# Optimization experiments

Hardware: AMD Instinct MI355X
Metric: run time of the kernel (lower is better)

## Reference

```python
import jax, jax.numpy as jnp
import numpy as np

B, L, E, H = 4, 512, 2048, 32
S = E // H  # head_size = 64
EXTRA_MAA, EXTRA_DECAY = 32, 64
EPS = 1e-5


def setup_inputs() -> dict:
    key = jax.random.key(0)
    ks = jax.random.split(key, 24)
    rn = lambda k, shp, s=1.0: jax.random.normal(k, shp, dtype=jnp.float32) * s
    return dict(
        x=rn(ks[0], (B, L, E)),
        state=rn(ks[1], (B, 2 + S, E), 0.1),
        ln1_w=jnp.ones((E,), jnp.float32), ln1_b=jnp.zeros((E,), jnp.float32),
        ln2_w=jnp.ones((E,), jnp.float32), ln2_b=jnp.zeros((E,), jnp.float32),
        maa_x=rn(ks[2], (E,), 0.02),
        maa_w1=rn(ks[3], (E, 5 * EXTRA_MAA), 0.02),
        maa_w2=rn(ks[4], (5, EXTRA_MAA, E), 0.02),
        maa_stack=rn(ks[5], (5, E), 0.02),          # [k,w,v,r,g] time_maa vectors
        time_decay=rn(ks[6], (E,), 0.5),
        decay_w1=rn(ks[7], (E, EXTRA_DECAY), 0.02),
        decay_w2=rn(ks[8], (EXTRA_DECAY, E), 0.02),
        faaaa=rn(ks[9], (H, S), 0.1),
        Wr=rn(ks[10], (E, E), 0.02), Wk=rn(ks[11], (E, E), 0.02),
        Wv=rn(ks[12], (E, E), 0.02), Wg=rn(ks[13], (E, E), 0.02),
        Wo=rn(ks[14], (E, E), 0.02),
        gn_w=jnp.ones((E,), jnp.float32), gn_b=jnp.zeros((E,), jnp.float32),
        ffn_maa_k=rn(ks[15], (E,), 0.02), ffn_maa_r=rn(ks[16], (E,), 0.02),
        ffn_Wk=rn(ks[17], (E, E), 0.02), ffn_Wr=rn(ks[18], (E, E), 0.02),
        ffn_Wv=rn(ks[19], (E, E), 0.02),
        i=0,
    )


def _ln(x, w, b):
    m = jnp.mean(x, axis=-1, keepdims=True)
    v = jnp.mean((x - m) ** 2, axis=-1, keepdims=True)
    return (x - m) * jax.lax.rsqrt(v + EPS) * w + b


def _token_shift(xn, prev_row):
    # sx_lerp[t] = x[t-1] - x[t], with state row as x[-1]
    first = (prev_row - xn[:, 0])[:, None]
    rest = xn[:, :-1] - xn[:, 1:]
    return jnp.concatenate([first, rest], axis=1)


def reference(x, state, ln1_w, ln1_b, ln2_w, ln2_b, maa_x, maa_w1, maa_w2,
              maa_stack, time_decay, decay_w1, decay_w2, faaaa,
              Wr, Wk, Wv, Wg, Wo, gn_w, gn_b,
              ffn_maa_k, ffn_maa_r, ffn_Wk, ffn_Wr, ffn_Wv, i):
    b, l = x.shape[0], x.shape[1]
    i0 = (2 + S) * i + 0
    i1 = (2 + S) * i + 1

    # ---- time mixing (parallel) ----
    xn = _ln(x, ln1_w, ln1_b)
    sx = _token_shift(xn, state[:, i1])
    xxx = jnp.tanh((xn + sx * maa_x) @ maa_w1).reshape(b, l, 5, 1, EXTRA_MAA)
    xxx = jnp.matmul(xxx, maa_w2).reshape(b, l, 5, E)   # [B,L,5,E]
    x5 = xn[:, :, None] + sx[:, :, None] * (maa_stack + xxx)

    w = jnp.exp(-jnp.exp(time_decay + jnp.tanh(x5[:, :, 1] @ decay_w1) @ decay_w2))
    w = w.reshape(b, l, H, S)
    r = (x5[:, :, 3] @ Wr.T).reshape(b, l, H, S)
    k = (x5[:, :, 0] @ Wk.T).reshape(b, l, H, S)
    v = (x5[:, :, 2] @ Wv.T).reshape(b, l, H, S)
    g = jax.nn.silu(x5[:, :, 4] @ Wg.T)                 # [B,L,E]

    s0 = state[:, (2 + S) * i + 2:(2 + S) * (i + 1)].reshape(b, H, S, S)
    u = faaaa[None, :, :, None]                         # [1,H,S,1]

    def step(s, rkvw):
        r_t, k_t, v_t, w_t = rkvw                      # each [B,H,S]
        a = k_t[:, :, :, None] * v_t[:, :, None, :]    # [B,H,S,S] outer product
        out = jnp.einsum('bhk,bhkd->bhd', r_t, u * a + s)
        return a + w_t[:, :, :, None] * s, out

    xs = tuple(jnp.moveaxis(t, 1, 0) for t in (r, k, v, w))
    _, outs = jax.lax.scan(step, s0, xs)               # outs [L,B,H,S]
    att = jnp.moveaxis(outs, 0, 1).reshape(b, l, E)

    # group norm over each head's channels
    a4 = att.reshape(b, l, H, S)
    m = jnp.mean(a4, axis=-1, keepdims=True)
    var = jnp.mean((a4 - m) ** 2, axis=-1, keepdims=True)
    att = ((a4 - m) * jax.lax.rsqrt(var + EPS)).reshape(b, l, E) * gn_w + gn_b
    x = x + (att * g) @ Wo.T

    # ---- channel mixing (parallel) ----
    xn2 = _ln(x, ln2_w, ln2_b)
    sx2 = _token_shift(xn2, state[:, i0])
    xk = xn2 + sx2 * ffn_maa_k
    xr = xn2 + sx2 * ffn_maa_r
    rr = jax.nn.sigmoid(xr @ ffn_Wr.T)
    kk = jnp.square(jax.nn.relu(xk @ ffn_Wk.T))
    x = x + rr * (kk @ ffn_Wv.T)
    return x
```

## Files before the change

kernel.cpp:

```cpp
#include <hip/hip_runtime.h>

#define EE 2048
#define LL 512
#define BBATCH 4
#define HH 32
#define SS 64
#define EPSF 1e-5f
static constexpr size_t NEL = (size_t)BBATCH * LL * EE;

typedef __attribute__((ext_vector_type(8))) short short8;
typedef __attribute__((ext_vector_type(4))) float f32x4;

__device__ __forceinline__ unsigned short f2bf(float f) {
  union { float f; unsigned u; } x; x.f = f;
  return (unsigned short)((x.u + 0x7fffu + ((x.u >> 16) & 1u)) >> 16);
}

__device__ __forceinline__ void gload_lds16(const unsigned short* g, unsigned short* l) {
  __builtin_amdgcn_global_load_lds((const __attribute__((address_space(1))) void*)g,
                                   (__attribute__((address_space(3))) void*)l, 16, 0, 0);
}

template <int N>
__device__ __forceinline__ void wait_vmcnt_n() {
  if constexpr (N == 4) asm volatile("s_waitcnt vmcnt(4)" ::: "memory");
  else if constexpr (N == 6) asm volatile("s_waitcnt vmcnt(6)" ::: "memory");
  else if constexpr (N == 8) asm volatile("s_waitcnt vmcnt(8)" ::: "memory");
  else asm volatile("s_waitcnt vmcnt(0)" ::: "memory");
}

struct CvArgs {
  const float* s[4];
  unsigned short* d[4];
};
__global__ void __launch_bounds__(256) f2bf_batch(CvArgs a, int n4) {
  int z = blockIdx.y;
  int idx = blockIdx.x * 256 + threadIdx.x;
  if (idx >= n4) return;
  float4 v = ((const float4*)a.s[z])[idx];
  ushort4 o;
  o.x = f2bf(v.x); o.y = f2bf(v.y); o.z = f2bf(v.z); o.w = f2bf(v.w);
  ((ushort4*)a.d[z])[idx] = o;
}

__global__ void __launch_bounds__(256) wprep_kernel(const float* __restrict__ w1,
                                                    const float* __restrict__ w2,
                                                    const float* __restrict__ d1,
                                                    const float* __restrict__ d2,
                                                    unsigned short* __restrict__ w1T,
                                                    unsigned short* __restrict__ w2cat,
                                                    unsigned short* __restrict__ dw1T,
                                                    unsigned short* __restrict__ dw2T) {
  const int N0 = 256 * 2048;
  const int N1 = 10240 * 160;
  const int N2 = 128 * 2048;
  const int N3 = 2048 * 128;
  int id = blockIdx.x * 256 + threadIdx.x;
  if (id < N0) {
    int n = id >> 11, k = id & 2047;
    float v = (n < 160) ? w1[(size_t)k * 160 + n] : 0.f;
    w1T[id] = f2bf(v);
    return;
  }
  id -= N0;
  if (id < N1) {
    int n = id / 160, kq = id - n * 160;
    int j = n >> 11, e = n & 2047;
    float v = ((kq >> 5) == j) ? w2[(size_t)kq * 2048 + e] : 0.f;
    w2cat[id] = f2bf(v);
    return;
  }
  id -= N1;
  if (id < N2) {
    int n = id >> 11, k = id & 2047;
    float v = (n < 64) ? d1[(size_t)k * 64 + n] : 0.f;
    dw1T[id] = f2bf(v);
    return;
  }
  id -= N2;
  if (id < N3) {
    int n = id >> 7, k = id & 127;
    float v = (k < 64) ? d2[(size_t)k * 2048 + n] : 0.f;
    dw2T[id] = f2bf(v);
  }
}

template <int SIDE>
__global__ void __launch_bounds__(256) ln_shift_kernel(
    const float* __restrict__ x, const float* __restrict__ state, const int* __restrict__ ip,
    const float* __restrict__ lnw, const float* __restrict__ lnb,
    const float* __restrict__ mA, const float* __restrict__ mB,
    float* __restrict__ xn_out, unsigned short* __restrict__ o1,
    float* __restrict__ sx_out, unsigned short* __restrict__ o2) {
  __shared__ float red[8];
  int tok = blockIdx.x;
  int b = tok >> 9, t = tok & 511;
  int tid = threadIdx.x;
  int e = tid * 8;
  size_t base = (size_t)tok * EE;
  float c[8], p[8];
  *(float4*)&c[0] = *(const float4*)&x[base + e];
  *(float4*)&c[4] = *(const float4*)&x[base + e + 4];
  bool hasp = (t != 0);
  if (hasp) {
    *(float4*)&p[0] = *(const float4*)&x[base - EE + e];
    *(float4*)&p[4] = *(const float4*)&x[base - EE + e + 4];
  } else {
    const float* srow = state + ((size_t)b * (2 + SS) + (size_t)(2 + SS) * (*ip) +
                                 (SIDE == 0 ? 1 : 0)) * EE;
    *(float4*)&p[0] = *(const float4*)&srow[e];
    *(float4*)&p[4] = *(const float4*)&srow[e + 4];
  }
  float sc = 0.f, sp = 0.f;
#pragma unroll
  for (int j = 0; j < 8; ++j) { sc += c[j]; sp += p[j]; }
#pragma unroll
  for (int off = 32; off >= 1; off >>= 1) {
    sc += __shfl_xor(sc, off);
    sp += __shfl_xor(sp, off);
  }
  if ((tid & 63) == 0) { red[tid >> 6] = sc; red[4 + (tid >> 6)] = sp; }
  __syncthreads();
  float mc = (red[0] + red[1] + red[2] + red[3]) * (1.f / EE);
  float mp = (red[4] + red[5] + red[6] + red[7]) * (1.f / EE);
  __syncthreads();
  float qc = 0.f, qp = 0.f;
#pragma unroll
  for (int j = 0; j < 8; ++j) {
    float dc = c[j] - mc, dp = p[j] - mp;
    qc += dc * dc; qp += dp * dp;
  }
#pragma unroll
  for (int off = 32; off >= 1; off >>= 1) {
    qc += __shfl_xor(qc, off);
    qp += __shfl_xor(qp, off);
  }
  if ((tid & 63) == 0) { red[tid >> 6] = qc; red[4 + (tid >> 6)] = qp; }
  __syncthreads();
  float rc = rsqrtf((red[0] + red[1] + red[2] + red[3]) * (1.f / EE) + EPSF);
  float rp = rsqrtf((red[4] + red[5] + red[6] + red[7]) * (1.f / EE) + EPSF);
  float wv[8], bv[8], av[8], bv2[8];
  *(float4*)&wv[0] = *(const float4*)&lnw[e];
  *(float4*)&wv[4] = *(const float4*)&lnw[e + 4];
  *(float4*)&bv[0] = *(const float4*)&lnb[e];
  *(float4*)&bv[4] = *(const float4*)&lnb[e + 4];
  *(float4*)&av[0] = *(const float4*)&mA[e];
  *(float4*)&av[4] = *(const float4*)&mA[e + 4];
  if (SIDE == 1) {
    *(float4*)&bv2[0] = *(const float4*)&mB[e];
    *(float4*)&bv2[4] = *(const float4*)&mB[e + 4];
  }
  float cn[8], sxv[8];
#pragma unroll
  for (int j = 0; j < 8; ++j) {
    float cnj = (c[j] - mc) * rc * wv[j] + bv[j];
    float pnj = hasp ? ((p[j] - mp) * rp * wv[j] + bv[j]) : p[j];
    cn[j] = cnj;
    sxv[j] = pnj - cnj;
  }
  if constexpr (SIDE == 0) {
    *(float4*)&xn_out[base + e] = *(float4*)&cn[0];
    *(float4*)&xn_out[base + e + 4] = *(float4*)&cn[4];
    *(float4*)&sx_out[base + e] = *(float4*)&sxv[0];
    *(float4*)&sx_out[base + e + 4] = *(float4*)&sxv[4];
    ushort4 xo0, xo1;
    xo0.x = f2bf(cn[0] + sxv[0] * av[0]); xo0.y = f2bf(cn[1] + sxv[1] * av[1]);
    xo0.z = f2bf(cn[2] + sxv[2] * av[2]); xo0.w = f2bf(cn[3] + sxv[3] * av[3]);
    xo1.x = f2bf(cn[4] + sxv[4] * av[4]); xo1.y = f2bf(cn[5] + sxv[5] * av[5]);
    xo1.z = f2bf(cn[6] + sxv[6] * av[6]); xo1.w = f2bf(cn[7] + sxv[7] * av[7]);
    *(ushort4*)&o1[base + e] = xo0;
    *(ushort4*)&o1[base + e + 4] = xo1;
  } else {
    ushort4 k0, k1, r0, r1;
    k0.x = f2bf(cn[0] + sxv[0] * av[0]); k0.y = f2bf(cn[1] + sxv[1] * av[1]);
    k0.z = f2bf(cn[2] + sxv[2] * av[2]); k0.w = f2bf(cn[3] + sxv[3] * av[3]);
    k1.x = f2bf(cn[4] + sxv[4] * av[4]); k1.y = f2bf(cn[5] + sxv[5] * av[5]);
    k1.z = f2bf(cn[6] + sxv[6] * av[6]); k1.w = f2bf(cn[7] + sxv[7] * av[7]);
    r0.x = f2bf(cn[0] + sxv[0] * bv2[0]); r0.y = f2bf(cn[1] + sxv[1] * bv2[1]);
    r0.z = f2bf(cn[2] + sxv[2] * bv2[2]); r0.w = f2bf(cn[3] + sxv[3] * bv2[3]);
    r1.x = f2bf(cn[4] + sxv[4] * bv2[4]); r1.y = f2bf(cn[5] + sxv[5] * bv2[5]);
    r1.z = f2bf(cn[6] + sxv[6] * bv2[6]); r1.w = f2bf(cn[7] + sxv[7] * bv2[7]);
    *(ushort4*)&o1[base + e] = k0;
    *(ushort4*)&o1[base + e + 4] = k1;
    *(ushort4*)&o2[base + e] = r0;
    *(ushort4*)&o2[base + e + 4] = r1;
  }
}

template <int ROWS, int BK>
__device__ __forceinline__ void stage_mat(const unsigned short* __restrict__ base, int ld,
                                          int k0, unsigned short* dst) {
  constexpr int GPR = BK / 8;
  constexpr int L = ROWS * GPR / 256;
  int tid = threadIdx.x;
#pragma unroll
  for (int r = 0; r < L; ++r) {
    int g = r * 256 + tid;
    int row = g / GPR, p = g & (GPR - 1);
    int lg = p ^ (row & (GPR - 1));
    gload_lds16(base + (size_t)row * ld + k0 + lg * 8, &dst[g * 8]);
  }
}

template <int BM, int BN, int BK>
__device__ __forceinline__ void gemm_core(const unsigned short* __restrict__ A, int lda,
                                          const unsigned short* __restrict__ W, int ldw,
                                          int K, int NB, unsigned short* AsAll,
                                          unsigned short* BsAll,
                                          f32x4 (&acc)[BM / 32][BN / 32], int& m0o, int& n0o) {
  constexpr int FM = BM / 32, FN = BN / 32, KS = BK / 32;
  constexpr int GPR = BK / 8;
  constexpr int NLD = (BM + BN) * GPR / 256;
  int nwg = gridDim.x, bid = blockIdx.x;
  int qd = nwg >> 3;
  int wg = (bid & 7) * qd + (bid >> 3);
  int bm = wg / NB, bn = wg - bm * NB;
  int tid = threadIdx.x;
  int wave = tid >> 6, lane = tid & 63;
  int wm = wave >> 1, wn = wave & 1;
  const unsigned short* Abase = A + (size_t)bm * BM * lda;
  const unsigned short* Bbase = W + (size_t)bn * BN * ldw;
  const int T = K / BK;
  stage_mat<BM, BK>(Abase, lda, 0, AsAll);
  stage_mat<BN, BK>(Bbase, ldw, 0, BsAll);
  {
    int k1 = (T > 1) ? BK : 0;
    stage_mat<BM, BK>(Abase, lda, k1, AsAll + BM * BK);
    stage_mat<BN, BK>(Bbase, ldw, k1, BsAll + BN * BK);
  }
  int q = lane >> 4;
  int rA = wm * (BM / 2) + (lane & 15);
  int rB = wn * (BN / 2) + (lane & 15);
  int xrA = rA & (GPR - 1), xrB = rB & (GPR - 1);
  for (int t = 0; t < T; ++t) {
    unsigned short* As = AsAll + (t & 1) * (BM * BK);
    unsigned short* Bs = BsAll + (t & 1) * (BN * BK);
    wait_vmcnt_n<NLD>();
    __builtin_amdgcn_s_barrier();
    __builtin_amdgcn_sched_barrier(0);
    __builtin_amdgcn_s_setprio(1);
    short8 av[KS][FM], bv[KS][FN];
#pragma unroll
    for (int ks = 0; ks < KS; ++ks) {
#pragma unroll
      for (int f = 0; f < FM; f++) {
        int p = (ks * 4 + q) ^ xrA;
        av[ks][f] = *(const short8*)&As[(rA + f * 16) * BK + p * 8];
      }
#pragma unroll
      for (int f = 0; f < FN; f++) {
        int p = (ks * 4 + q) ^ xrB;
        bv[ks][f] = *(const short8*)&Bs[(rB + f * 16) * BK + p * 8];
      }
    }
#pragma unroll
    for (int ks = 0; ks < KS; ++ks)
#pragma unroll
      for (int fm = 0; fm < FM; fm++)
#pragma unroll
        for (int fn = 0; fn < FN; fn++)
          acc[fm][fn] = __builtin_amdgcn_mfma_f32_16x16x32_bf16(av[ks][fm], bv[ks][fn],
                                                                acc[fm][fn], 0, 0, 0);
    __builtin_amdgcn_s_setprio(0);
    asm volatile("s_waitcnt lgkmcnt(0)" ::: "memory");
    __builtin_amdgcn_sched_barrier(0);
    __builtin_amdgcn_s_barrier();
    int tn = t + 2;
    if (tn >= T) tn -= T;
    stage_mat<BM, BK>(Abase, lda, tn * BK, As);
    stage_mat<BN, BK>(Bbase, ldw, tn * BK, Bs);
  }
  m0o = bm * BM + wm * (BM / 2);
  n0o = bn * BN + wn * (BN / 2);
}

template <int FM, int FN, typename F>
__device__ __forceinline__ void epi_loop(f32x4 (&acc)[FM][FN], int m0, int n0, F f) {
  int lane = threadIdx.x & 63;
  int rl = (lane >> 4) * 4, cl = lane & 15;
#pragma unroll
  for (int fm = 0; fm < FM; fm++)
#pragma unroll
    for (int fn = 0; fn < FN; fn++)
#pragma unroll
      for (int q = 0; q < 4; q++)
        f(m0 + fm * 16 + rl + q, n0 + fn * 16 + cl, acc[fm][fn][q]);
}

template <int MODE, int BM, int BN, int BK>
__global__ void __launch_bounds__(256) gemm_bt(const unsigned short* __restrict__ A, int lda,
                                               const unsigned short* __restrict__ W, int ldw,
                                               int K, int NB, void* __restrict__ Cout, int ldc,
                                               const float* __restrict__ p1,
                                               const float* __restrict__ p2,
                                               const float* __restrict__ p3) {
  __shared__ __align__(16) unsigned short As[2 * BM * BK];
  __shared__ __align__(16) unsigned short Bs[2 * BN * BK];
  f32x4 acc[BM / 32][BN / 32] = {};
  int m0, n0;
  gemm_core<BM, BN, BK>(A, lda, W, ldw, K, NB, As, Bs, acc, m0, n0);
  epi_loop(acc, m0, n0, [&](int m, int n, float val) {
    size_t o = (size_t)m * ldc + n;
    if constexpr (MODE == 2) {
      ((float*)Cout)[o] = p1[o] + val;
    } else if constexpr (MODE == 3) {
      ((float*)Cout)[o] = p1[o] + val * (1.f / (1.f + expf(-p2[o])));
    } else if constexpr (MODE == 5) {
      ((unsigned short*)Cout)[o] = f2bf(tanhf(val));
    } else if constexpr (MODE == 6) {
      ((float*)Cout)[o] = expf(-expf(p1[n] + val));
    } else {
      int j = n >> 11, e = n & 2047;
      size_t oe = (size_t)m * EE + e;
      float xv = p1[oe];
      float sv = p2[oe];
      float st = p3[(size_t)j * EE + e];
      ((unsigned short*)Cout)[(size_t)j * NEL + oe] = f2bf(xv + sv * (st + val));
    }
  });
}

struct Proj4Args {
  const unsigned short* A[4];
  const unsigned short* W[4];
  float* C[4];
};
__global__ void __launch_bounds__(256) gemm_proj4(Proj4Args args) {
  __shared__ __align__(16) unsigned short As[2 * 128 * 64];
  __shared__ __align__(16) unsigned short Bs[2 * 128 * 64];
  int z = blockIdx.y;
  f32x4 acc[4][4] = {};
  int m0, n0;
  gemm_core<128, 128, 64>(args.A[z], EE, args.W[z], EE, EE, 16, As, Bs, acc, m0, n0);
  float* C = args.C[z];
  bool silu = (z == 3);
  epi_loop(acc, m0, n0, [&](int m, int n, float val) {
    size_t o = (size_t)m * EE + n;
    C[o] = silu ? (val / (1.f + expf(-val))) : val;
  });
}

__global__ void __launch_bounds__(256) gemm_ffn2(const unsigned short* A0,
                                                 const unsigned short* A1,
                                                 const unsigned short* W0,
                                                 const unsigned short* W1, float* C0,
                                                 unsigned short* C1) {
  __shared__ __align__(16) unsigned short As[2 * 128 * 64];
  __shared__ __align__(16) unsigned short Bs[2 * 128 * 64];
  int z = blockIdx.y;
  f32x4 acc[4][4] = {};
  int m0, n0;
  gemm_core<128, 128, 64>(z ? A1 : A0, EE, z ? W1 : W0, EE, EE, 16, As, Bs, acc, m0, n0);
  epi_loop(acc, m0, n0, [&](int m, int n, float val) {
    size_t o = (size_t)m * EE + n;
    if (z == 0) {
      C0[o] = val;
    } else {
      float rv = fmaxf(val, 0.f);
      C1[o] = f2bf(rv * rv);
    }
  });
}

__global__ void __launch_bounds__(512) scan_kernel(const float* __restrict__ r,
                                                   const float* __restrict__ k,
                                                   const float* __restrict__ v,
                                                   const float* __restrict__ w,
                                                   const float* __restrict__ state,
                                                   const float* __restrict__ faaaa,
                                                   const int* __restrict__ ip,
                                                   float* __restrict__ att) {
  __shared__ float bR[2][8][32], bK[2][8][32], bW[2][8][32];
  __shared__ float bV[2][8][64];
  __shared__ float part[8][8][64];
  int blk = blockIdx.x;
  int bh = blk >> 1, kh = blk & 1;
  int b = bh >> 5, h = bh & 31;
  int tid = threadIdx.x, wv = tid >> 6, lane = tid & 63;
  int klocal = wv * 4;
  int k0w = kh * 32 + klocal;
  int ii = *ip;
  const float* sb = state + ((size_t)b * (2 + SS) + (size_t)(2 + SS) * ii + 2) * EE;
  float s_[4], u_[4];
#pragma unroll
  for (int q = 0; q < 4; ++q) {
    int kk_ = k0w + q;
    s_[q] = sb[(size_t)(2 * h + (kk_ >> 5)) * EE + (kk_ & 31) * 64 + lane];
    u_[q] = faaaa[h * 64 + kk_];
  }
  size_t base = (size_t)b * LL * EE + (size_t)h * 64;
  int c = tid;
  bool ld = c < 320;
  int lt = c / 40, r40 = c - lt * 40;
  int la = (r40 < 24) ? (r40 >> 3) : 3;
  int lcG = (r40 < 24) ? (kh * 32 + (r40 & 7) * 4) : ((r40 - 24) * 4);
  int lcL = (r40 < 24) ? ((r40 & 7) * 4) : ((r40 - 24) * 4);
  const float* lsrc = nullptr;
  if (ld) {
    const float* arr = (la == 0) ? r : (la == 1) ? k : (la == 2) ? w : v;
    lsrc = arr + base + (size_t)lt * EE + lcG;
    float4 v0 = *(const float4*)lsrc;
    if (la == 0) *(float4*)&bR[0][lt][lcL] = v0;
    else if (la == 1) *(float4*)&bK[0][lt][lcL] = v0;
    else if (la == 2) *(float4*)&bW[0][lt][lcL] = v0;
    else *(float4*)&bV[0][lt][lcL] = v0;
  }
  __syncthreads();
  for (int g = 0; g < 64; ++g) {
    int cb = g & 1;
    float4 nv;
    if (ld && g < 63) nv = *(const float4*)(lsrc + (size_t)(g + 1) * 8 * EE);
#pragma unroll
    for (int t = 0; t < 8; ++t) {
      float vv = bV[cb][t][lane];
      float acc = 0.f;
#pragma unroll
      for (int q = 0; q < 4; ++q) {
        float rk = bR[cb][t][klocal + q];
        float kk2 = bK[cb][t][klocal + q];
        float wk = bW[cb][t][klocal + q];
        float a = kk2 * vv;
        acc = fmaf(rk, fmaf(u_[q], a, s_[q]), acc);
        s_[q] = fmaf(wk, s_[q], a);
      }
      part[t][wv][lane] = acc;
    }
    if (ld && g < 63) {
      int nb = cb ^ 1;
      if (la == 0) *(float4*)&bR[nb][lt][lcL] = nv;
      else if (la == 1) *(float4*)&bK[nb][lt][lcL] = nv;
      else if (la == 2) *(float4*)&bW[nb][lt][lcL] = nv;
      else *(float4*)&bV[nb][lt][lcL] = nv;
    }
    __syncthreads();
    {
      int t = tid >> 6, d = tid & 63;
      float tot = part[t][0][d] + part[t][1][d] + part[t][2][d] + part[t][3][d] +
                  part[t][4][d] + part[t][5][d] + part[t][6][d] + part[t][7][d];
      atomicAdd(&att[base + (size_t)(g * 8 + t) * EE + d], tot);
    }
    __syncthreads();
  }
}

__global__ void __launch_bounds__(256) gn_gate_kernel(const float* __restrict__ att,
                                                      const float* __restrict__ g,
                                                      const float* __restrict__ gnw,
                                                      const float* __restrict__ gnb,
                                                      unsigned short* __restrict__ attg) {
  int tok = blockIdx.x, tid = threadIdx.x;
  int h = tid >> 3, j = tid & 7;
  size_t base = (size_t)tok * EE + h * 64 + j * 8;
  int e = h * 64 + j * 8;
  float4 a0 = *(const float4*)&att[base];
  float4 a1 = *(const float4*)&att[base + 4];
  float s = a0.x + a0.y + a0.z + a0.w + a1.x + a1.y + a1.z + a1.w;
  s += __shfl_xor(s, 1); s += __shfl_xor(s, 2); s += __shfl_xor(s, 4);
  float mean = s * (1.f / 64.f);
  float d, q = 0.f;
  d = a0.x - mean; q += d * d; d = a0.y - mean; q += d * d;
  d = a0.z - mean; q += d * d; d = a0.w - mean; q += d * d;
  d = a1.x - mean; q += d * d; d = a1.y - mean; q += d * d;
  d = a1.z - mean; q += d * d; d = a1.w - mean; q += d * d;
  q += __shfl_xor(q, 1); q += __shfl_xor(q, 2); q += __shfl_xor(q, 4);
  float rstd = rsqrtf(q * (1.f / 64.f) + EPSF);
  float4 w0 = *(const float4*)&gnw[e], w1 = *(const float4*)&gnw[e + 4];
  float4 b0 = *(const float4*)&gnb[e], b1 = *(const float4*)&gnb[e + 4];
  float4 g0 = *(const float4*)&g[base], g1 = *(const float4*)&g[base + 4];
  ushort4 o0, o1;
  o0.x = f2bf(((a0.x - mean) * rstd * w0.x + b0.x) * g0.x);
  o0.y = f2bf(((a0.y - mean) * rstd * w0.y + b0.y) * g0.y);
  o0.z = f2bf(((a0.z - mean) * rstd * w0.z + b0.z) * g0.z);
  o0.w = f2bf(((a0.w - mean) * rstd * w0.w + b0.w) * g0.w);
  o1.x = f2bf(((a1.x - mean) * rstd * w1.x + b1.x) * g1.x);
  o1.y = f2bf(((a1.y - mean) * rstd * w1.y + b1.y) * g1.y);
  o1.z = f2bf(((a1.z - mean) * rstd * w1.z + b1.z) * g1.z);
  o1.w = f2bf(((a1.w - mean) * rstd * w1.w + b1.w) * g1.w);
  *(ushort4*)&attg[base] = o0;
  *(ushort4*)&attg[base + 4] = o1;
}

extern "C" void kernel_launch(void* const* d_in, const int* in_sizes, int n_in,
                              void* d_out, int out_size, void* d_ws, size_t ws_size,
                              hipStream_t stream) {
  const float* x = (const float*)d_in[0];
  const float* state = (const float*)d_in[1];
  const float* ln1_w = (const float*)d_in[2];
  const float* ln1_b = (const float*)d_in[3];
  const float* ln2_w = (const float*)d_in[4];
  const float* ln2_b = (const float*)d_in[5];
  const float* maa_x = (const float*)d_in[6];
  const float* maa_w1 = (const float*)d_in[7];
  const float* maa_w2 = (const float*)d_in[8];
  const float* maa_stack = (const float*)d_in[9];
  const float* time_decay = (const float*)d_in[10];
  const float* decay_w1 = (const float*)d_in[11];
  const float* decay_w2 = (const float*)d_in[12];
  const float* faaaa = (const float*)d_in[13];
  const float* Wr = (const float*)d_in[14];
  const float* Wk = (const float*)d_in[15];
  const float* Wv = (const float*)d_in[16];
  const float* Wg = (const float*)d_in[17];
  const float* Wo = (const float*)d_in[18];
  const float* gn_w = (const float*)d_in[19];
  const float* gn_b = (const float*)d_in[20];
  const float* ffn_maa_k = (const float*)d_in[21];
  const float* ffn_maa_r = (const float*)d_in[22];
  const float* fWk = (const float*)d_in[23];
  const float* fWr = (const float*)d_in[24];
  const float* fWv = (const float*)d_in[25];
  const int* ip = (const int*)d_in[26];

  char* ws = (char*)d_ws;
  const size_t MB1 = 1024 * 1024;
  unsigned short* WB0 = (unsigned short*)ws;
  unsigned short* WB1 = (unsigned short*)(ws + 8 * MB1);
  float* xn = (float*)(ws + 16 * MB1);
  unsigned short* x5b = (unsigned short*)(ws + 32 * MB1);
  float* wbuf = (float*)(ws + 72 * MB1);
  float* rbuf = (float*)(ws + 88 * MB1);
  float* kbuf = (float*)(ws + 104 * MB1);
  float* vbuf = (float*)(ws + 120 * MB1);
  float* gbuf = (float*)(ws + 136 * MB1);
  char* smalls = ws + 152 * MB1;
  unsigned short* th = (unsigned short*)smalls;
  unsigned short* w1T = (unsigned short*)(smalls + 1 * MB1);
  unsigned short* w2cat = (unsigned short*)(smalls + 2 * MB1);
  unsigned short* dw1T = (unsigned short*)(smalls + 5376 * 1024);
  unsigned short* dw2T = (unsigned short*)(smalls + 5888 * 1024);
  unsigned short* dt = (unsigned short*)(smalls + 6400 * 1024);

  unsigned short* xxm = (unsigned short*)wbuf;
  float* sx = gbuf;
  float* att = xn;
  unsigned short* WB2 = (unsigned short*)xn;
  unsigned short* WB3 = WB2 + NEL;
  unsigned short* attg = x5b;
  unsigned short* xkb = x5b + 1 * NEL;
  unsigned short* xrb = x5b + 2 * NEL;
  unsigned short* kkb = x5b + 3 * NEL;
  unsigned short* fWkB = x5b + 4 * NEL;
  unsigned short* fWvB = (unsigned short*)kbuf;
  float* rrraw = wbuf;

  const int thr = 256;
  const int nconv = (int)(NEL / 4);

  ln_shift_kernel<0><<<BBATCH * LL, thr, 0, stream>>>(x, state, ip, ln1_w, ln1_b, maa_x,
                                                      nullptr, xn, xxm, sx, nullptr);
  wprep_kernel<<<10496, thr, 0, stream>>>(maa_w1, maa_w2, decay_w1, decay_w2, w1T, w2cat,
                                          dw1T, dw2T);
  gemm_bt<5, 64, 64, 64><<<128, thr, 0, stream>>>(xxm, 2048, w1T, 2048, 2048, 4, th, 256,
                                                  nullptr, nullptr, nullptr);
  gemm_bt<7, 128, 128, 32><<<1280, thr, 0, stream>>>(th, 256, w2cat, 160, 160, 80, x5b, 0,
                                                     xn, sx, maa_stack);
  gemm_bt<5, 64, 64, 64><<<64, thr, 0, stream>>>(x5b + 1 * NEL, 2048, dw1T, 2048, 2048, 2,
                                                 dt, 128, nullptr, nullptr, nullptr);
  gemm_bt<6, 128, 128, 64><<<256, thr, 0, stream>>>(dt, 128, dw2T, 128, 128, 16, wbuf, 2048,
                                                    time_decay, nullptr, nullptr);
  {
    CvArgs ca;
    ca.s[0] = Wk; ca.d[0] = WB0;
    ca.s[1] = Wv; ca.d[1] = WB1;
    ca.s[2] = Wr; ca.d[2] = WB2;
    ca.s[3] = Wg; ca.d[3] = WB3;
    f2bf_batch<<<dim3(4096, 4), thr, 0, stream>>>(ca, nconv);
  }
  {
    Proj4Args pa;
    pa.A[0] = x5b + 0 * NEL; pa.W[0] = WB0; pa.C[0] = kbuf;
    pa.A[1] = x5b + 2 * NEL; pa.W[1] = WB1; pa.C[1] = vbuf;
    pa.A[2] = x5b + 3 * NEL; pa.W[2] = WB2; pa.C[2] = rbuf;
    pa.A[3] = x5b + 4 * NEL; pa.W[3] = WB3; pa.C[3] = gbuf;
    gemm_proj4<<<dim3(256, 4), thr, 0, stream>>>(pa);
  }
  {
    CvArgs cb;
    cb.s[0] = Wo; cb.d[0] = WB0;
    cb.s[1] = fWr; cb.d[1] = WB1;
    cb.s[2] = fWk; cb.d[2] = fWkB;
    cb.s[3] = fWk; cb.d[3] = fWkB;
    f2bf_batch<<<dim3(4096, 3), thr, 0, stream>>>(cb, nconv);
  }
  (void)hipMemsetAsync(att, 0, NEL * sizeof(float), stream);
  scan_kernel<<<256, 512, 0, stream>>>(rbuf, kbuf, vbuf, wbuf, state, faaaa, ip, att);
  {
    CvArgs cc;
    cc.s[0] = fWv; cc.d[0] = fWvB;
    cc.s[1] = fWv; cc.d[1] = fWvB;
    cc.s[2] = fWv; cc.d[2] = fWvB;
    cc.s[3] = fWv; cc.d[3] = fWvB;
    f2bf_batch<<<dim3(4096, 1), thr, 0, stream>>>(cc, nconv);
  }
  gn_gate_kernel<<<BBATCH * LL, thr, 0, stream>>>(att, gbuf, gn_w, gn_b, attg);
  gemm_bt<2, 128, 64, 64><<<512, thr, 0, stream>>>(attg, 2048, WB0, 2048, 2048, 32,
                                                   (float*)d_out, 2048, x, nullptr, nullptr);
  ln_shift_kernel<1><<<BBATCH * LL, thr, 0, stream>>>((const float*)d_out, state, ip, ln2_w,
                                                      ln2_b, ffn_maa_k, ffn_maa_r, nullptr,
                                                      xkb, nullptr, xrb);
  gemm_ffn2<<<dim3(256, 2), thr, 0, stream>>>(xrb, xkb, WB1, fWkB, rrraw, kkb);
  gemm_bt<3, 128, 64, 64><<<512, thr, 0, stream>>>(kkb, 2048, fWvB, 2048, 2048, 32,
                                                   (float*)d_out, 2048, (const float*)d_out,
                                                   rrraw, nullptr);
}
```

Measured before the change: 463.8 us.

## Issue next-tile loads before MFMAs, XCD-aware batched GEMM tiling, merge weight conversion

Inside the GEMM main loop, the MFMA block now runs after the next tile's global-to-LDS loads are issued, so the loads overlap with compute instead of following it. The batched projection and FFN GEMMs switch from a 2D grid to a 1D grid. Each XCD is mapped to one matrix (or half of one), so blocks that share A/W data land on the same L2. The separate fWv conversion launch is folded into the earlier batch conversion, and buffer aliasing is rearranged so fWvB and xkb stay valid across the scan.

```diff
diff --git a/kernel.cpp b/kernel.cpp
--- a/kernel.cpp
+++ b/kernel.cpp
@@ -205,16 +205,12 @@
 template <int BM, int BN, int BK>
 __device__ __forceinline__ void gemm_core(const unsigned short* __restrict__ A, int lda,
                                           const unsigned short* __restrict__ W, int ldw,
-                                          int K, int NB, unsigned short* AsAll,
+                                          int K, int bm, int bn, unsigned short* AsAll,
                                           unsigned short* BsAll,
                                           f32x4 (&acc)[BM / 32][BN / 32], int& m0o, int& n0o) {
   constexpr int FM = BM / 32, FN = BN / 32, KS = BK / 32;
   constexpr int GPR = BK / 8;
   constexpr int NLD = (BM + BN) * GPR / 256;
-  int nwg = gridDim.x, bid = blockIdx.x;
-  int qd = nwg >> 3;
-  int wg = (bid & 7) * qd + (bid >> 3);
-  int bm = wg / NB, bn = wg - bm * NB;
   int tid = threadIdx.x;
   int wave = tid >> 6, lane = tid & 63;
   int wm = wave >> 1, wn = wave & 1;
@@ -238,7 +234,6 @@
     wait_vmcnt_n<NLD>();
     __builtin_amdgcn_s_barrier();
     __builtin_amdgcn_sched_barrier(0);
-    __builtin_amdgcn_s_setprio(1);
     short8 av[KS][FM], bv[KS][FN];
 #pragma unroll
     for (int ks = 0; ks < KS; ++ks) {
@@ -253,15 +248,6 @@
         bv[ks][f] = *(const short8*)&Bs[(rB + f * 16) * BK + p * 8];
       }
     }
-#pragma unroll
-    for (int ks = 0; ks < KS; ++ks)
-#pragma unroll
-      for (int fm = 0; fm < FM; fm++)
-#pragma unroll
-        for (int fn = 0; fn < FN; fn++)
-          acc[fm][fn] = __builtin_amdgcn_mfma_f32_16x16x32_bf16(av[ks][fm], bv[ks][fn],
-                                                                acc[fm][fn], 0, 0, 0);
-    __builtin_amdgcn_s_setprio(0);
     asm volatile("s_waitcnt lgkmcnt(0)" ::: "memory");
     __builtin_amdgcn_sched_barrier(0);
     __builtin_amdgcn_s_barrier();
@@ -269,6 +255,16 @@
     if (tn >= T) tn -= T;
     stage_mat<BM, BK>(Abase, lda, tn * BK, As);
     stage_mat<BN, BK>(Bbase, ldw, tn * BK, Bs);
+    __builtin_amdgcn_s_setprio(1);
+#pragma unroll
+    for (int ks = 0; ks < KS; ++ks)
+#pragma unroll
+      for (int fm = 0; fm < FM; fm++)
+#pragma unroll
+        for (int fn = 0; fn < FN; fn++)
+          acc[fm][fn] = __builtin_amdgcn_mfma_f32_16x16x32_bf16(av[ks][fm], bv[ks][fn],
+                                                                acc[fm][fn], 0, 0, 0);
+    __builtin_amdgcn_s_setprio(0);
   }
   m0o = bm * BM + wm * (BM / 2);
   n0o = bn * BN + wn * (BN / 2);
@@ -296,9 +292,13 @@
                                                const float* __restrict__ p3) {
   __shared__ __align__(16) unsigned short As[2 * BM * BK];
   __shared__ __align__(16) unsigned short Bs[2 * BN * BK];
+  int nwg = gridDim.x, bid = blockIdx.x;
+  int qd = nwg >> 3;
+  int wg = (bid & 7) * qd + (bid >> 3);
+  int bm = wg / NB, bn = wg - bm * NB;
   f32x4 acc[BM / 32][BN / 32] = {};
   int m0, n0;
-  gemm_core<BM, BN, BK>(A, lda, W, ldw, K, NB, As, Bs, acc, m0, n0);
+  gemm_core<BM, BN, BK>(A, lda, W, ldw, K, bm, bn, As, Bs, acc, m0, n0);
   epi_loop(acc, m0, n0, [&](int m, int n, float val) {
     size_t o = (size_t)m * ldc + n;
     if constexpr (MODE == 2) {
@@ -328,10 +328,14 @@
 __global__ void __launch_bounds__(256) gemm_proj4(Proj4Args args) {
   __shared__ __align__(16) unsigned short As[2 * 128 * 64];
   __shared__ __align__(16) unsigned short Bs[2 * 128 * 64];
-  int z = blockIdx.y;
+  int bid = blockIdx.x;
+  int xcd = bid & 7;
+  int z = xcd >> 1;
+  int tile = ((xcd & 1) << 7) + (bid >> 3);
+  int bm = tile >> 4, bn = tile & 15;
   f32x4 acc[4][4] = {};
   int m0, n0;
-  gemm_core<128, 128, 64>(args.A[z], EE, args.W[z], EE, EE, 16, As, Bs, acc, m0, n0);
+  gemm_core<128, 128, 64>(args.A[z], EE, args.W[z], EE, EE, bm, bn, As, Bs, acc, m0, n0);
   float* C = args.C[z];
   bool silu = (z == 3);
   epi_loop(acc, m0, n0, [&](int m, int n, float val) {
@@ -347,10 +351,14 @@
                                                  unsigned short* C1) {
   __shared__ __align__(16) unsigned short As[2 * 128 * 64];
   __shared__ __align__(16) unsigned short Bs[2 * 128 * 64];
-  int z = blockIdx.y;
+  int bid = blockIdx.x;
+  int xcd = bid & 7;
+  int z = xcd >> 2;
+  int tile = ((xcd & 3) << 6) + (bid >> 3);
+  int bm = tile >> 4, bn = tile & 15;
   f32x4 acc[4][4] = {};
   int m0, n0;
-  gemm_core<128, 128, 64>(z ? A1 : A0, EE, z ? W1 : W0, EE, EE, 16, As, Bs, acc, m0, n0);
+  gemm_core<128, 128, 64>(z ? A1 : A0, EE, z ? W1 : W0, EE, EE, bm, bn, As, Bs, acc, m0, n0);
   epi_loop(acc, m0, n0, [&](int m, int n, float val) {
     size_t o = (size_t)m * EE + n;
     if (z == 0) {
@@ -536,11 +544,11 @@
   unsigned short* WB2 = (unsigned short*)xn;
   unsigned short* WB3 = WB2 + NEL;
   unsigned short* attg = x5b;
-  unsigned short* xkb = x5b + 1 * NEL;
+  unsigned short* xkb = x5b;
+  unsigned short* fWvB = x5b + 1 * NEL;
   unsigned short* xrb = x5b + 2 * NEL;
   unsigned short* kkb = x5b + 3 * NEL;
   unsigned short* fWkB = x5b + 4 * NEL;
-  unsigned short* fWvB = (unsigned short*)kbuf;
   float* rrraw = wbuf;
 
   const int thr = 256;
@@ -572,33 +580,25 @@
     pa.A[1] = x5b + 2 * NEL; pa.W[1] = WB1; pa.C[1] = vbuf;
     pa.A[2] = x5b + 3 * NEL; pa.W[2] = WB2; pa.C[2] = rbuf;
     pa.A[3] = x5b + 4 * NEL; pa.W[3] = WB3; pa.C[3] = gbuf;
-    gemm_proj4<<<dim3(256, 4), thr, 0, stream>>>(pa);
+    gemm_proj4<<<1024, thr, 0, stream>>>(pa);
   }
   {
     CvArgs cb;
     cb.s[0] = Wo; cb.d[0] = WB0;
     cb.s[1] = fWr; cb.d[1] = WB1;
     cb.s[2] = fWk; cb.d[2] = fWkB;
-    cb.s[3] = fWk; cb.d[3] = fWkB;
-    f2bf_batch<<<dim3(4096, 3), thr, 0, stream>>>(cb, nconv);
+    cb.s[3] = fWv; cb.d[3] = fWvB;
+    f2bf_batch<<<dim3(4096, 4), thr, 0, stream>>>(cb, nconv);
   }
   (void)hipMemsetAsync(att, 0, NEL * sizeof(float), stream);
   scan_kernel<<<256, 512, 0, stream>>>(rbuf, kbuf, vbuf, wbuf, state, faaaa, ip, att);
-  {
-    CvArgs cc;
-    cc.s[0] = fWv; cc.d[0] = fWvB;
-    cc.s[1] = fWv; cc.d[1] = fWvB;
-    cc.s[2] = fWv; cc.d[2] = fWvB;
-    cc.s[3] = fWv; cc.d[3] = fWvB;
-    f2bf_batch<<<dim3(4096, 1), thr, 0, stream>>>(cc, nconv);
-  }
   gn_gate_kernel<<<BBATCH * LL, thr, 0, stream>>>(att, gbuf, gn_w, gn_b, attg);
   gemm_bt<2, 128, 64, 64><<<512, thr, 0, stream>>>(attg, 2048, WB0, 2048, 2048, 32,
                                                    (float*)d_out, 2048, x, nullptr, nullptr);
   ln_shift_kernel<1><<<BBATCH * LL, thr, 0, stream>>>((const float*)d_out, state, ip, ln2_w,
                                                       ln2_b, ffn_maa_k, ffn_maa_r, nullptr,
                                                       xkb, nullptr, xrb);
-  gemm_ffn2<<<dim3(256, 2), thr, 0, stream>>>(xrb, xkb, WB1, fWkB, rrraw, kkb);
+  gemm_ffn2<<<512, thr, 0, stream>>>(xrb, xkb, WB1, fWkB, rrraw, kkb);
   gemm_bt<3, 128, 64, 64><<<512, thr, 0, stream>>>(kkb, 2048, fWvB, 2048, 2048, 32,
                                                    (float*)d_out, 2048, (const float*)d_out,
                                                    rrraw, nullptr);
```

Result: faster. 441.4 us (-4.8%).
